# Optimization experiments

Hardware: AMD Instinct MI355X
Metric: run time of the kernel (lower is better)

## Reference

```python
import jax, jax.numpy as jnp
import numpy as np

BSZ, SEQ, DIM = 2, 2048, 4096
N_HEADS, N_KV_HEADS, HEAD_DIM = 32, 8, 128
N_REP = N_HEADS // N_KV_HEADS
MAX_BS, MAX_SEQ = 4, 2048
ROPE_THETA = 500000.0


def setup_inputs() -> dict:
    key = jax.random.key(0)
    ks = jax.random.split(key, 6)
    sc = 1.0 / np.sqrt(DIM)
    x = jax.random.normal(ks[0], (BSZ, SEQ, DIM), jnp.float32)
    wq = jax.random.normal(ks[1], (DIM, N_HEADS * HEAD_DIM), jnp.float32) * sc
    wk = jax.random.normal(ks[2], (DIM, N_KV_HEADS * HEAD_DIM), jnp.float32) * sc
    wv = jax.random.normal(ks[3], (DIM, N_KV_HEADS * HEAD_DIM), jnp.float32) * sc
    wo = jax.random.normal(ks[4], (N_HEADS * HEAD_DIM, DIM), jnp.float32) * sc
    cache_k = jnp.zeros((MAX_BS, MAX_SEQ, N_KV_HEADS, HEAD_DIM), jnp.float32)
    cache_v = jnp.zeros((MAX_BS, MAX_SEQ, N_KV_HEADS, HEAD_DIM), jnp.float32)
    # precomputed rotary frequencies (freqs_cis = cos + i*sin)
    inv = 1.0 / (ROPE_THETA ** (np.arange(0, HEAD_DIM, 2, dtype=np.float32) / HEAD_DIM))
    t = np.arange(SEQ, dtype=np.float32)
    freqs = np.outer(t, inv)  # [SEQ, HEAD_DIM//2]
    freqs_cos = jnp.asarray(np.cos(freqs), jnp.float32)
    freqs_sin = jnp.asarray(np.sin(freqs), jnp.float32)
    # causal additive mask, broadcast over (batch, heads)
    neg = jnp.full((SEQ, SEQ), -1e9, jnp.float32)
    mask = jnp.triu(neg, k=1)[None, None, :, :]
    return {"x": x, "wq": wq, "wk": wk, "wv": wv, "wo": wo,
            "cache_k": cache_k, "cache_v": cache_v,
            "freqs_cos": freqs_cos, "freqs_sin": freqs_sin,
            "mask": mask, "start_pos": 0}


def _apply_rope(t, cos, sin):
    # t: [b, s, h, d]; complex multiply on (even, odd) pairs
    b, s, h, d = t.shape
    tr = t.reshape(b, s, h, d // 2, 2)
    a, bb = tr[..., 0], tr[..., 1]
    cos = cos[None, :, None, :]
    sin = sin[None, :, None, :]
    out = jnp.stack([a * cos - bb * sin, a * sin + bb * cos], axis=-1)
    return out.reshape(b, s, h, d)


def reference(x, wq, wk, wv, wo, cache_k, cache_v, freqs_cos, freqs_sin, mask, start_pos):
    bsz, seqlen, _ = x.shape
    xq = (x @ wq).reshape(bsz, seqlen, N_HEADS, HEAD_DIM)
    xk = (x @ wk).reshape(bsz, seqlen, N_KV_HEADS, HEAD_DIM)
    xv = (x @ wv).reshape(bsz, seqlen, N_KV_HEADS, HEAD_DIM)
    xq = _apply_rope(xq, freqs_cos, freqs_sin)
    xk = _apply_rope(xk, freqs_cos, freqs_sin)
    # KV-cache append (start_pos is a static Python int)
    cache_k = jax.lax.dynamic_update_slice(cache_k, xk, (0, start_pos, 0, 0))
    cache_v = jax.lax.dynamic_update_slice(cache_v, xv, (0, start_pos, 0, 0))
    keys = cache_k[:bsz, : start_pos + seqlen]    # [b, kv_len, kvh, d]
    values = cache_v[:bsz, : start_pos + seqlen]
    # GQA repeat_kv: tile kv heads n_rep times -> [b, kv_len, H, d]
    keys = jnp.repeat(keys, N_REP, axis=2)
    values = jnp.repeat(values, N_REP, axis=2)
    q = xq.transpose(0, 2, 1, 3)        # [b, H, s, d]
    k = keys.transpose(0, 2, 1, 3)      # [b, H, kv, d]
    v = values.transpose(0, 2, 1, 3)
    scores = jnp.einsum('bhqd,bhkd->bhqk', q, k) / np.sqrt(HEAD_DIM)
    if mask is not None:
        scores = scores + mask
    probs = jax.nn.softmax(scores.astype(jnp.float32), axis=-1).astype(q.dtype)
    out = jnp.einsum('bhqk,bhkd->bhqd', probs, v)
    out = out.transpose(0, 2, 1, 3).reshape(bsz, seqlen, -1)
    return out @ wo
```

## Files before the change

kernel.cpp:

```cpp
#include <hip/hip_runtime.h>
#include <hip/hip_bf16.h>
#include <cstdint>

typedef __attribute__((ext_vector_type(8))) __bf16 bf16x8;
typedef __attribute__((ext_vector_type(4))) __bf16 bf16x4;
typedef __attribute__((ext_vector_type(2))) __bf16 bf16x2;
typedef __attribute__((ext_vector_type(4))) float  f32x4;

#define MFMA16(a,b,c) __builtin_amdgcn_mfma_f32_16x16x32_bf16((a),(b),(c),0,0,0)

__device__ __forceinline__ void gl16(const void* g, void* l) {
  __builtin_amdgcn_global_load_lds(
      (const __attribute__((address_space(1))) void*)g,
      (__attribute__((address_space(3))) void*)l, 16, 0, 0);
}

static constexpr int BSZ = 2, SEQ = 2048, DIM = 4096;
static constexpr int NH = 32, NKV = 8, HD = 128;
static constexpr int TOK = BSZ * SEQ;
static constexpr int NQKV = NH*HD + 2*NKV*HD;
static constexpr float QSCALE = 0.08838834764831845f;
static constexpr float FNEG = -3.0e38f;

__global__ __launch_bounds__(256) void f32_to_bf16_k(const float* __restrict__ in,
                                                     __bf16* __restrict__ out) {
  int i = (blockIdx.x * 256 + threadIdx.x) * 4;
  float4 v = *(const float4*)(in + i);
  bf16x4 o = { (__bf16)v.x, (__bf16)v.y, (__bf16)v.z, (__bf16)v.w };
  *(bf16x4*)(out + i) = o;
}

__global__ __launch_bounds__(256) void wtrans64_k(const float* __restrict__ S,
                                                  __bf16* __restrict__ D, int sC) {
  __shared__ __align__(16) __bf16 t[64 * 66];
  const int tid = threadIdx.x;
  const int cb = blockIdx.x, rb = blockIdx.y;
#pragma unroll
  for (int i = 0; i < 16; ++i) {
    int e = i * 256 + tid; int r = e >> 6, c = e & 63;
    t[c * 66 + r] = (__bf16)S[(size_t)(rb * 64 + r) * sC + cb * 64 + c];
  }
  __syncthreads();
#pragma unroll
  for (int i = 0; i < 16; ++i) {
    int e = i * 256 + tid; int c = e >> 6, r = e & 63;
    D[(size_t)(cb * 64 + c) * 4096 + rb * 64 + r] = t[c * 66 + r];
  }
}

template<int M, int N, int K>
__global__ __launch_bounds__(256, 2) void gemm2p_k(const __bf16* __restrict__ A,
                                                   const __bf16* __restrict__ Bt,
                                                   float* __restrict__ C) {
  __shared__ __align__(16) __bf16 lA[2][128 * 64];
  __shared__ __align__(16) __bf16 lB[2][128 * 64];
  constexpr int NBX = N / 128;
  constexpr int NWG = (M / 128) * NBX;
  const int lin = blockIdx.x;
  const int swz = (lin & 7) * (NWG / 8) + (lin >> 3);
  const int bm = swz / NBX, bn = swz % NBX;
  const int tid = threadIdx.x, lane = tid & 63, wid = tid >> 6;
  const int wm = wid & 1, wn = wid >> 1;
  const int lo = lane & 15, hi = lane >> 4;
  f32x4 acc[4][4] = {};

  const int srow = lane >> 3, scol = lane & 7;
  const __bf16* Ag = A + ((size_t)bm * 128 + wid * 8 + srow) * K + scol * 8;
  const __bf16* Bg = Bt + ((size_t)bn * 128 + wid * 8 + srow) * K + scol * 8;

  auto STAGE = [&](int kt) {
    __bf16* dA = lA[kt & 1] + wid * 512;
    __bf16* dB = lB[kt & 1] + wid * 512;
    const __bf16* ag = Ag + (size_t)kt * 64;
    const __bf16* bg = Bg + (size_t)kt * 64;
#pragma unroll
    for (int i = 0; i < 4; ++i) {
      gl16(ag + (size_t)i * 32 * K, dA + i * 2048);
      gl16(bg + (size_t)i * 32 * K, dB + i * 2048);
    }
  };

  constexpr int NK = K / 64;
  STAGE(0);
  __syncthreads();

  for (int kt = 0; kt < NK; ++kt) {
    if (kt + 1 < NK) STAGE(kt + 1);
    const __bf16* bA = lA[kt & 1];
    const __bf16* bB = lB[kt & 1];
#pragma unroll
    for (int kk = 0; kk < 2; ++kk) {
      bf16x8 af[4], bfv[4];
#pragma unroll
      for (int m = 0; m < 4; ++m)
        af[m] = *(const bf16x8*)&bA[(wm * 64 + m * 16 + lo) * 64 + kk * 32 + hi * 8];
#pragma unroll
      for (int n = 0; n < 4; ++n)
        bfv[n] = *(const bf16x8*)&bB[(wn * 64 + n * 16 + lo) * 64 + kk * 32 + hi * 8];
      __builtin_amdgcn_s_setprio(1);
#pragma unroll
      for (int m = 0; m < 4; ++m)
#pragma unroll
        for (int n = 0; n < 4; ++n)
          acc[m][n] = MFMA16(af[m], bfv[n], acc[m][n]);
      __builtin_amdgcn_s_setprio(0);
    }
    __syncthreads();
  }

  const int r0 = hi * 4, cN = lo;
#pragma unroll
  for (int m = 0; m < 4; ++m) {
    size_t row = (size_t)bm * 128 + wm * 64 + m * 16 + r0;
#pragma unroll
    for (int n = 0; n < 4; ++n) {
      size_t col = (size_t)bn * 128 + wn * 64 + n * 16 + cN;
#pragma unroll
      for (int r = 0; r < 4; ++r)
        C[(row + r) * N + col] = acc[m][n][r];
    }
  }
}

__global__ __launch_bounds__(256) void rope_qk_k(const float* __restrict__ QKV,
                                                 const float* __restrict__ fc,
                                                 const float* __restrict__ fs,
                                                 __bf16* __restrict__ Qb,
                                                 __bf16* __restrict__ Kb) {
  int idx = blockIdx.x * 256 + threadIdx.x;
  int tok = idx / 2560;
  int rem = idx - tok * 2560;
  int head = rem >> 6, p = rem & 63;
  int b = tok >> 11, s = tok & 2047;
  float2 v = *(const float2*)(QKV + (size_t)tok * NQKV + head * 128 + 2 * p);
  float c = fc[s * 64 + p], sn = fs[s * 64 + p];
  float x = v.x * c - v.y * sn;
  float y = v.x * sn + v.y * c;
  if (head < 32) {
    x *= QSCALE; y *= QSCALE;
    bf16x2 o = { (__bf16)x, (__bf16)y };
    *(bf16x2*)(Qb + ((size_t)(b * 32 + head) * 2048 + s) * 128 + 2 * p) = o;
  } else {
    bf16x2 o = { (__bf16)x, (__bf16)y };
    *(bf16x2*)(Kb + ((size_t)(b * 8 + head - 32) * 2048 + s) * 128 + 2 * p) = o;
  }
}

__global__ __launch_bounds__(256) void vtrans_k(const float* __restrict__ QKV,
                                                __bf16* __restrict__ Vt) {
  __shared__ __align__(16) __bf16 t[128 * 66];
  const int sb = blockIdx.x, hk = blockIdx.y, b = blockIdx.z;
  const int tid = threadIdx.x;
#pragma unroll
  for (int i = 0; i < 32; ++i) {
    int e = i * 256 + tid; int s = e >> 7, d = e & 127;
    t[d * 66 + s] = (__bf16)QKV[(size_t)(b * 2048 + sb * 64 + s) * NQKV + 5120 + hk * 128 + d];
  }
  __syncthreads();
  int d = tid >> 1, s0 = (tid & 1) * 32;
  __bf16* dst = Vt + ((size_t)(b * 8 + hk) * 128 + d) * 2048 + sb * 64 + s0;
  const unsigned* srcu = (const unsigned*)&t[d * 66 + s0];
  unsigned* dstu = (unsigned*)dst;
#pragma unroll
  for (int i = 0; i < 16; ++i) dstu[i] = srcu[i];
}

__global__ __launch_bounds__(256, 2) void attn128_k(const __bf16* __restrict__ Q,
                                                    const __bf16* __restrict__ Kc,
                                                    const __bf16* __restrict__ Vt,
                                                    __bf16* __restrict__ Ab) {
  __shared__ __align__(16) __bf16 lK[2][64 * 128];
  __shared__ __align__(16) __bf16 lV[2][128 * 64];
  __shared__ __align__(16) __bf16 lP[4][16 * 64];
  const int qt = gridDim.x - 1 - blockIdx.x;
  const int h = blockIdx.y, b = blockIdx.z;
  const int hk = h >> 2;
  const int tid = threadIdx.x, lane = tid & 63, wid = tid >> 6;
  const int qb = qt * 128;
  const int lo = lane & 15, hi = lane >> 4;
  const int xk = (lo & 7) * 8;
  const int srow8 = lane >> 3, scol8 = lane & 7;
  const __bf16* Qp = Q + ((size_t)(b * 32 + h) * 2048 + qb) * 128;
  const __bf16* Kp = Kc + (size_t)(b * 8 + hk) * 2048 * 128;
  const __bf16* Vp = Vt + (size_t)(b * 8 + hk) * 128 * 2048;

  bf16x8 qf[2][4];
#pragma unroll
  for (int rt = 0; rt < 2; ++rt)
#pragma unroll
    for (int kq = 0; kq < 4; ++kq)
      qf[rt][kq] = *(const bf16x8*)(Qp + (size_t)(rt * 64 + wid * 16 + lo) * 128 + kq * 32 + hi * 8);

  f32x4 accO[2][8] = {};
  float mr[2][4] = { { FNEG, FNEG, FNEG, FNEG }, { FNEG, FNEG, FNEG, FNEG } };
  float lr[2][4] = {};

  const int nkb = 2 * qt + 2;

  auto STAGE = [&](int t) {
    const int kbase = t * 64;
    __bf16* dK = lK[t & 1];
    __bf16* dV = lV[t & 1];
#pragma unroll
    for (int i = 0; i < 4; ++i) {
      const int krow = (i * 4 + wid) * 4 + hi;
      gl16(Kp + (size_t)(kbase + krow) * 128 + (lo ^ (krow & 7)) * 8,
           dK + (i * 4 + wid) * 512);
      const int vrow = (i * 4 + wid) * 8 + srow8;
      gl16(Vp + (size_t)vrow * 2048 + kbase + (scol8 ^ srow8) * 8,
           dV + (i * 4 + wid) * 512);
    }
  };

  STAGE(0);
  asm volatile("s_waitcnt vmcnt(0)" ::: "memory");
  __builtin_amdgcn_s_barrier();

  for (int kb = 0; kb < nkb; ++kb) {
    const int cur = kb & 1;
    if (kb + 1 < nkb) STAGE(kb + 1);
    const bool maskb = (kb >= nkb - 2);
    const __bf16* bK = lK[cur];
    const __bf16* bV = lV[cur];

#pragma unroll
    for (int rt = 0; rt < 2; ++rt) {
      f32x4 sc[4] = {};
      __builtin_amdgcn_s_setprio(1);
#pragma unroll
      for (int nb = 0; nb < 4; ++nb)
#pragma unroll
        for (int kk = 0; kk < 4; ++kk) {
          bf16x8 kf = *(const bf16x8*)&bK[(nb * 16 + lo) * 128 + ((kk * 32 + hi * 8) ^ xk)];
          sc[nb] = MFMA16(qf[rt][kk], kf, sc[nb]);
        }
      __builtin_amdgcn_s_setprio(0);

      const int qrow0 = qb + rt * 64 + wid * 16 + hi * 4;
      const int kcol0 = kb * 64 + lo;
      float tm[4] = { FNEG, FNEG, FNEG, FNEG };
#pragma unroll
      for (int nb = 0; nb < 4; ++nb)
#pragma unroll
        for (int r = 0; r < 4; ++r) {
          float s = sc[nb][r];
          if (maskb && (kcol0 + nb * 16 > qrow0 + r)) s = FNEG;
          sc[nb][r] = s;
          tm[r] = fmaxf(tm[r], s);
        }
#pragma unroll
      for (int r = 0; r < 4; ++r) {
#pragma unroll
        for (int off = 1; off < 16; off <<= 1)
          tm[r] = fmaxf(tm[r], __shfl_xor(tm[r], off));
        float mn = fmaxf(mr[rt][r], tm[r]);
        tm[r] = __expf(mr[rt][r] - mn);
        mr[rt][r] = mn;
      }
      float rs[4] = {};
#pragma unroll
      for (int nb = 0; nb < 4; ++nb)
#pragma unroll
        for (int r = 0; r < 4; ++r) {
          float p = __expf(sc[nb][r] - mr[rt][r]);
          rs[r] += p;
          const int q = hi * 4 + r;
          lP[wid][q * 64 + ((nb * 16 + lo) ^ ((q & 7) * 8))] = (__bf16)p;
        }
#pragma unroll
      for (int r = 0; r < 4; ++r) {
#pragma unroll
        for (int off = 1; off < 16; off <<= 1)
          rs[r] += __shfl_xor(rs[r], off);
        lr[rt][r] = lr[rt][r] * tm[r] + rs[r];
      }
#pragma unroll
      for (int nb2 = 0; nb2 < 8; ++nb2)
#pragma unroll
        for (int r = 0; r < 4; ++r)
          accO[rt][nb2][r] *= tm[r];

      __builtin_amdgcn_s_setprio(1);
#pragma unroll
      for (int kk = 0; kk < 2; ++kk) {
        bf16x8 pf = *(const bf16x8*)&lP[wid][lo * 64 + ((kk * 32 + hi * 8) ^ xk)];
#pragma unroll
        for (int nb2 = 0; nb2 < 8; ++nb2) {
          bf16x8 vf = *(const bf16x8*)&bV[(nb2 * 16 + lo) * 64 + ((kk * 32 + hi * 8) ^ xk)];
          accO[rt][nb2] = MFMA16(pf, vf, accO[rt][nb2]);
        }
      }
      __builtin_amdgcn_s_setprio(0);
    }

    if (kb + 1 < nkb) asm volatile("s_waitcnt vmcnt(0)" ::: "memory");
    __builtin_amdgcn_s_barrier();
  }

#pragma unroll
  for (int rt = 0; rt < 2; ++rt) {
    float inv[4];
#pragma unroll
    for (int r = 0; r < 4; ++r) inv[r] = 1.0f / lr[rt][r];
#pragma unroll
    for (int nb2 = 0; nb2 < 8; ++nb2)
#pragma unroll
      for (int r = 0; r < 4; ++r)
        Ab[((size_t)b * 2048 + qb + rt * 64 + wid * 16 + hi * 4 + r) * 4096 + h * 128 + nb2 * 16 + lo] =
            (__bf16)(accO[rt][nb2][r] * inv[r]);
  }
}

extern "C" void kernel_launch(void* const* d_in, const int* in_sizes, int n_in,
                              void* d_out, int out_size, void* d_ws, size_t ws_size,
                              hipStream_t stream) {
  const float* x  = (const float*)d_in[0];
  const float* wq = (const float*)d_in[1];
  const float* wk = (const float*)d_in[2];
  const float* wv = (const float*)d_in[3];
  const float* wo = (const float*)d_in[4];
  const float* fc = (const float*)d_in[7];
  const float* fs = (const float*)d_in[8];
  float* out = (float*)d_out;

  char* ws = (char*)d_ws;
  __bf16* Wqkvt = (__bf16*)(ws + 0);
  __bf16* Wot   = (__bf16*)(ws + 50331648);
  __bf16* Qb    = (__bf16*)(ws + 83886080);
  __bf16* Kb    = (__bf16*)(ws + 117440512);
  __bf16* Vtb   = (__bf16*)(ws + 125829120);
  __bf16* Xbf   = (__bf16*)(ws + 134217728);
  float*  QKVf  = (float*)(ws + 167772160);
  __bf16* Ab    = (__bf16*)(ws + 167772160);

  f32_to_bf16_k<<<TOK * DIM / 1024, 256, 0, stream>>>(x, Xbf);
  wtrans64_k<<<dim3(64, 64), 256, 0, stream>>>(wq, Wqkvt, 4096);
  wtrans64_k<<<dim3(16, 64), 256, 0, stream>>>(wk, Wqkvt + (size_t)4096 * 4096, 1024);
  wtrans64_k<<<dim3(16, 64), 256, 0, stream>>>(wv, Wqkvt + (size_t)5120 * 4096, 1024);
  wtrans64_k<<<dim3(64, 64), 256, 0, stream>>>(wo, Wot, 4096);

  gemm2p_k<4096, 6144, 4096><<<1536, 256, 0, stream>>>(Xbf, Wqkvt, QKVf);

  rope_qk_k<<<TOK * 40 * 64 / 256, 256, 0, stream>>>(QKVf, fc, fs, Qb, Kb);
  vtrans_k<<<dim3(32, 8, 2), 256, 0, stream>>>(QKVf, Vtb);

  attn128_k<<<dim3(16, 32, 2), 256, 0, stream>>>(Qb, Kb, Vtb, Ab);

  gemm2p_k<4096, 4096, 4096><<<1024, 256, 0, stream>>>(Ab, Wot, out);
}
```

Baseline: 1.106 ms.

## Rework GEMM into triple-buffered K=32 pipeline with XOR-swizzled LDS

Replaces the double-buffered K=64 GEMM with a three-stage K=32 pipeline. It uses explicit vmcnt waits and raw barriers, so each iteration waits only for the older tile and keeps two loads in flight. LDS rows are XOR-swizzled to avoid bank conflicts on the fragment reads, and occupancy is raised to 3 workgroups per CU. The L2-friendly block swizzle is dropped in favour of plain row-major block order, which may hurt cache reuse.

```diff
diff --git a/kernel.cpp b/kernel.cpp
--- a/kernel.cpp
+++ b/kernel.cpp
@@ -49,63 +49,67 @@
 }
 
 template<int M, int N, int K>
-__global__ __launch_bounds__(256, 2) void gemm2p_k(const __bf16* __restrict__ A,
+__global__ __launch_bounds__(256, 3) void gemm3p_k(const __bf16* __restrict__ A,
                                                    const __bf16* __restrict__ Bt,
                                                    float* __restrict__ C) {
-  __shared__ __align__(16) __bf16 lA[2][128 * 64];
-  __shared__ __align__(16) __bf16 lB[2][128 * 64];
+  __shared__ __align__(16) __bf16 lA[3][128 * 32];
+  __shared__ __align__(16) __bf16 lB[3][128 * 32];
   constexpr int NBX = N / 128;
-  constexpr int NWG = (M / 128) * NBX;
   const int lin = blockIdx.x;
-  const int swz = (lin & 7) * (NWG / 8) + (lin >> 3);
-  const int bm = swz / NBX, bn = swz % NBX;
+  const int bm = lin / NBX, bn = lin % NBX;
   const int tid = threadIdx.x, lane = tid & 63, wid = tid >> 6;
   const int wm = wid & 1, wn = wid >> 1;
   const int lo = lane & 15, hi = lane >> 4;
   f32x4 acc[4][4] = {};
 
-  const int srow = lane >> 3, scol = lane & 7;
-  const __bf16* Ag = A + ((size_t)bm * 128 + wid * 8 + srow) * K + scol * 8;
-  const __bf16* Bg = Bt + ((size_t)bn * 128 + wid * 8 + srow) * K + scol * 8;
-
-  auto STAGE = [&](int kt) {
-    __bf16* dA = lA[kt & 1] + wid * 512;
-    __bf16* dB = lB[kt & 1] + wid * 512;
-    const __bf16* ag = Ag + (size_t)kt * 64;
-    const __bf16* bg = Bg + (size_t)kt * 64;
-#pragma unroll
-    for (int i = 0; i < 4; ++i) {
-      gl16(ag + (size_t)i * 32 * K, dA + i * 2048);
-      gl16(bg + (size_t)i * 32 * K, dB + i * 2048);
+  const int srow = wid * 16 + (lane >> 2);
+  const int schunk = (lane & 3) ^ ((lane >> 2) & 3) ^ ((lane >> 4) & 3);
+  const __bf16* Ag = A + (size_t)(bm * 128) * K;
+  const __bf16* Bg = Bt + (size_t)(bn * 128) * K;
+
+  auto STAGE = [&](int kt, int bsel) {
+    const int kcol = kt * 32;
+#pragma unroll
+    for (int i = 0; i < 2; ++i) {
+      gl16(Ag + (size_t)(i * 64 + srow) * K + kcol + schunk * 8,
+           &lA[bsel][(i * 64 + wid * 16) * 32]);
+      gl16(Bg + (size_t)(i * 64 + srow) * K + kcol + schunk * 8,
+           &lB[bsel][(i * 64 + wid * 16) * 32]);
     }
   };
 
-  constexpr int NK = K / 64;
-  STAGE(0);
-  __syncthreads();
-
+  constexpr int NK = K / 32;
+  STAGE(0, 0);
+  STAGE(1, 1);
+  asm volatile("s_waitcnt vmcnt(4)" ::: "memory");
+  __builtin_amdgcn_s_barrier();
+
+  const int rswA = (lo & 3) ^ ((lo >> 2) & 3);
+  int bsel = 0, bnx = 2;
   for (int kt = 0; kt < NK; ++kt) {
-    if (kt + 1 < NK) STAGE(kt + 1);
-    const __bf16* bA = lA[kt & 1];
-    const __bf16* bB = lB[kt & 1];
-#pragma unroll
-    for (int kk = 0; kk < 2; ++kk) {
-      bf16x8 af[4], bfv[4];
-#pragma unroll
-      for (int m = 0; m < 4; ++m)
-        af[m] = *(const bf16x8*)&bA[(wm * 64 + m * 16 + lo) * 64 + kk * 32 + hi * 8];
+    const bool more = (kt + 2 < NK);
+    if (more) STAGE(kt + 2, bnx);
+    const __bf16* bA = lA[bsel];
+    const __bf16* bB = lB[bsel];
+    bf16x8 af[4], bfv[4];
+#pragma unroll
+    for (int m = 0; m < 4; ++m)
+      af[m] = *(const bf16x8*)&bA[(wm * 64 + m * 16 + lo) * 32 + ((hi ^ rswA) * 8)];
+#pragma unroll
+    for (int n = 0; n < 4; ++n)
+      bfv[n] = *(const bf16x8*)&bB[(wn * 64 + n * 16 + lo) * 32 + ((hi ^ rswA) * 8)];
+    __builtin_amdgcn_s_setprio(1);
+#pragma unroll
+    for (int m = 0; m < 4; ++m)
 #pragma unroll
       for (int n = 0; n < 4; ++n)
-        bfv[n] = *(const bf16x8*)&bB[(wn * 64 + n * 16 + lo) * 64 + kk * 32 + hi * 8];
-      __builtin_amdgcn_s_setprio(1);
-#pragma unroll
-      for (int m = 0; m < 4; ++m)
-#pragma unroll
-        for (int n = 0; n < 4; ++n)
-          acc[m][n] = MFMA16(af[m], bfv[n], acc[m][n]);
-      __builtin_amdgcn_s_setprio(0);
-    }
-    __syncthreads();
+        acc[m][n] = MFMA16(af[m], bfv[n], acc[m][n]);
+    __builtin_amdgcn_s_setprio(0);
+    if (more) asm volatile("s_waitcnt vmcnt(4)" ::: "memory");
+    else      asm volatile("s_waitcnt vmcnt(0)" ::: "memory");
+    __builtin_amdgcn_s_barrier();
+    bsel = (bsel == 2) ? 0 : bsel + 1;
+    bnx  = (bnx == 2) ? 0 : bnx + 1;
   }
 
   const int r0 = hi * 4, cN = lo;
@@ -339,12 +343,12 @@
   wtrans64_k<<<dim3(16, 64), 256, 0, stream>>>(wv, Wqkvt + (size_t)5120 * 4096, 1024);
   wtrans64_k<<<dim3(64, 64), 256, 0, stream>>>(wo, Wot, 4096);
 
-  gemm2p_k<4096, 6144, 4096><<<1536, 256, 0, stream>>>(Xbf, Wqkvt, QKVf);
+  gemm3p_k<4096, 6144, 4096><<<1536, 256, 0, stream>>>(Xbf, Wqkvt, QKVf);
 
   rope_qk_k<<<TOK * 40 * 64 / 256, 256, 0, stream>>>(QKVf, fc, fs, Qb, Kb);
   vtrans_k<<<dim3(32, 8, 2), 256, 0, stream>>>(QKVf, Vtb);
 
   attn128_k<<<dim3(16, 32, 2), 256, 0, stream>>>(Qb, Kb, Vtb, Ab);
 
-  gemm2p_k<4096, 4096, 4096><<<1024, 256, 0, stream>>>(Ab, Wot, out);
-}
+  gemm3p_k<4096, 4096, 4096><<<1024, 256, 0, stream>>>(Ab, Wot, out);
+}
```

Result: faster. 1.045 ms (-5.6%).
